# Performance work log

Measured on AMD Instinct MI355X. Metric: run time of the kernel, lower is better.

The kernel has to match this reference:

```python
import jax, jax.numpy as jnp
import numpy as np

ALPHA = 0.2  # LeakyReLU negative slope


def setup_inputs() -> dict:
    key = jax.random.key(0)
    k1, k2, k3, k4 = jax.random.split(key, 4)
    N, IN, OUT = 8192, 512, 256
    x = jax.random.normal(k1, (N, IN), dtype=jnp.float32)
    adj = jnp.zeros((N, N), dtype=jnp.float32)  # accepted but unused by the module
    W = jax.random.normal(k2, (OUT, IN), dtype=jnp.float32) * (1.0 / np.sqrt(IN))
    a1 = jax.random.normal(k3, (OUT,), dtype=jnp.float32) * (1.0 / np.sqrt(OUT))
    a2 = jax.random.normal(k4, (OUT,), dtype=jnp.float32) * (1.0 / np.sqrt(OUT))
    return {"x": x, "adj": adj, "W": W, "a1": a1, "a2": a2}


def reference(x, adj, W, a1, a2):
    # h = tran(x): [N, OUT]
    h = x @ W.T
    # additive GAT scores: e[i, j] = a2 . h_i + a1 . h_j  (from unsqueeze(0)+unsqueeze(1))
    s1 = h @ a1  # [N], att1(h)
    s2 = h @ a2  # [N], att2(h)
    e = s2[:, None] + s1[None, :]  # [N, N]
    e = jnp.where(e > 0, e, ALPHA * e)  # LeakyReLU
    attn = jax.nn.softmax(e, axis=1)  # softmax over dim=1; dropout is identity in eval
    return attn @ h  # [N, OUT]
```

## Files before the change

kernel.cpp:

```cpp
#include <hip/hip_runtime.h>

#define NROW 8192
#define DIN  512
#define DOUT 256
#define NCHUNK 256
#define CLEN 32

constexpr size_t OFF_H      = 0;
constexpr size_t OFF_S1     = OFF_H + (size_t)NROW*DOUT*4;
constexpr size_t OFF_S2     = OFF_S1 + NROW*4;
constexpr size_t OFF_RANK   = OFF_S2 + NROW*4;
constexpr size_t OFF_MISC   = OFF_RANK + NROW*4;
constexpr size_t MEMSET_LEN = OFF_MISC + 256 - OFF_S1;
constexpr size_t OFF_S1S    = OFF_MISC + 256;
constexpr size_t OFF_PERM   = OFF_S1S + NROW*4;
constexpr size_t OFF_WHI    = OFF_PERM + NROW*4;
constexpr size_t OFF_WLO    = OFF_WHI + NROW*4;
constexpr size_t OFF_PRELOS = OFF_WLO + NROW*4;
constexpr size_t OFF_SUFHIS = OFF_PRELOS + 33024;
constexpr size_t OFF_CSLO   = OFF_SUFHIS + 33024;
constexpr size_t OFF_CSHI   = OFF_CSLO + 1024;
constexpr size_t OFF_TLO    = OFF_CSHI + 1024;
constexpr size_t OFF_THI    = OFF_TLO + (size_t)NCHUNK*DOUT*4;
constexpr size_t OFF_PRELO  = OFF_THI + (size_t)NCHUNK*DOUT*4;
constexpr size_t OFF_SUFHI  = OFF_PRELO + (size_t)(NROW+1)*DOUT*4;
constexpr size_t WS_NEED    = OFF_SUFHI + (size_t)(NROW+1)*DOUT*4;

typedef float f32x4 __attribute__((ext_vector_type(4)));
typedef short s16x8 __attribute__((ext_vector_type(8)));
typedef unsigned int u32x4 __attribute__((ext_vector_type(4)));

__device__ __forceinline__ void cvt8_pair(const float4 u, const float4 v,
                                          s16x8& hi, s16x8& lo) {
  float f[8] = {u.x, u.y, u.z, u.w, v.x, v.y, v.z, v.w};
  u32x4 hp, lp;
#pragma unroll
  for (int p = 0; p < 4; ++p) {
    const float f0 = f[2 * p], f1 = f[2 * p + 1];
    const unsigned b0 = __float_as_uint(f0);
    const unsigned b1 = __float_as_uint(f1);
    hp[p] = __builtin_amdgcn_perm(b1, b0, 0x07060302u);
    const float r0 = f0 - __uint_as_float(b0 & 0xffff0000u);
    const float r1 = f1 - __uint_as_float(b1 & 0xffff0000u);
    lp[p] = __builtin_amdgcn_perm(__float_as_uint(r1), __float_as_uint(r0), 0x07060302u);
  }
  hi = __builtin_bit_cast(s16x8, hp);
  lo = __builtin_bit_cast(s16x8, lp);
}

__global__ __launch_bounds__(256) void gemm_h_mfma(const float* __restrict__ x,
                                                   const float* __restrict__ W,
                                                   const float* __restrict__ a1,
                                                   const float* __restrict__ a2,
                                                   float* __restrict__ h,
                                                   float* __restrict__ s1,
                                                   float* __restrict__ s2) {
  __shared__ unsigned short AsH[64][72], AsL[64][72], BsH[64][72], BsL[64][72];
  const int tid = threadIdx.x;
  const int bid = blockIdx.x;
  const int swz = (bid & 7) * 64 + (bid >> 3);
  const int rowBase = (swz >> 2) * 64;
  const int colBase = (swz & 3) * 64;
  const int wid = tid >> 6, lane = tid & 63;
  const int wRow = wid >> 1, wCol = wid & 1;
  const int lhi = lane >> 4, llo = lane & 15;

  f32x4 acc[2][2];
#pragma unroll
  for (int m = 0; m < 2; ++m)
#pragma unroll
    for (int n = 0; n < 2; ++n) acc[m][n] = (f32x4)(0.f);

  const int tr = tid >> 2;
  const int tq = tid & 3;
  const float* px = x + (size_t)(rowBase + tr) * DIN + tq * 16;
  const float* pw = W + (size_t)(colBase + tr) * DIN + tq * 16;

  s16x8 cAh[2], cAl[2], cBh[2], cBl[2];
  {
    float4 a0 = *(const float4*)(px + 0),  a1v = *(const float4*)(px + 4);
    float4 a2v = *(const float4*)(px + 8), a3 = *(const float4*)(px + 12);
    float4 b0 = *(const float4*)(pw + 0),  b1 = *(const float4*)(pw + 4);
    float4 b2 = *(const float4*)(pw + 8),  b3 = *(const float4*)(pw + 12);
    cvt8_pair(a0, a1v, cAh[0], cAl[0]);
    cvt8_pair(a2v, a3, cAh[1], cAl[1]);
    cvt8_pair(b0, b1, cBh[0], cBl[0]);
    cvt8_pair(b2, b3, cBh[1], cBl[1]);
  }

  for (int k0 = 0; k0 < DIN; k0 += 64) {
    __syncthreads();
    *(s16x8*)&AsH[tr][tq * 16 + 0] = cAh[0];
    *(s16x8*)&AsH[tr][tq * 16 + 8] = cAh[1];
    *(s16x8*)&AsL[tr][tq * 16 + 0] = cAl[0];
    *(s16x8*)&AsL[tr][tq * 16 + 8] = cAl[1];
    *(s16x8*)&BsH[tr][tq * 16 + 0] = cBh[0];
    *(s16x8*)&BsH[tr][tq * 16 + 8] = cBh[1];
    *(s16x8*)&BsL[tr][tq * 16 + 0] = cBl[0];
    *(s16x8*)&BsL[tr][tq * 16 + 8] = cBl[1];
    __syncthreads();
    const bool more = (k0 + 64 < DIN);
    float4 a0, a1v, a2v, a3, b0, b1, b2, b3;
    if (more) {
      a0 = *(const float4*)(px + k0 + 64 + 0);  a1v = *(const float4*)(px + k0 + 64 + 4);
      a2v = *(const float4*)(px + k0 + 64 + 8); a3 = *(const float4*)(px + k0 + 64 + 12);
      b0 = *(const float4*)(pw + k0 + 64 + 0);  b1 = *(const float4*)(pw + k0 + 64 + 4);
      b2 = *(const float4*)(pw + k0 + 64 + 8);  b3 = *(const float4*)(pw + k0 + 64 + 12);
    }
#pragma unroll
    for (int kk = 0; kk < 64; kk += 32) {
      s16x8 afh[2], afl[2], bfh[2], bfl[2];
#pragma unroll
      for (int m = 0; m < 2; ++m) {
        afh[m] = *(const s16x8*)&AsH[wRow * 32 + m * 16 + llo][kk + lhi * 8];
        afl[m] = *(const s16x8*)&AsL[wRow * 32 + m * 16 + llo][kk + lhi * 8];
      }
#pragma unroll
      for (int n = 0; n < 2; ++n) {
        bfh[n] = *(const s16x8*)&BsH[wCol * 32 + n * 16 + llo][kk + lhi * 8];
        bfl[n] = *(const s16x8*)&BsL[wCol * 32 + n * 16 + llo][kk + lhi * 8];
      }
#pragma unroll
      for (int m = 0; m < 2; ++m)
#pragma unroll
        for (int n = 0; n < 2; ++n) {
          acc[m][n] = __builtin_amdgcn_mfma_f32_16x16x32_bf16(afh[m], bfh[n], acc[m][n], 0, 0, 0);
          acc[m][n] = __builtin_amdgcn_mfma_f32_16x16x32_bf16(afl[m], bfh[n], acc[m][n], 0, 0, 0);
          acc[m][n] = __builtin_amdgcn_mfma_f32_16x16x32_bf16(afh[m], bfl[n], acc[m][n], 0, 0, 0);
        }
    }
    if (more) {
      cvt8_pair(a0, a1v, cAh[0], cAl[0]);
      cvt8_pair(a2v, a3, cAh[1], cAl[1]);
      cvt8_pair(b0, b1, cBh[0], cBl[0]);
      cvt8_pair(b2, b3, cBh[1], cBl[1]);
    }
  }
  float a1c[2], a2c[2];
#pragma unroll
  for (int n = 0; n < 2; ++n) {
    const int col = colBase + wCol * 32 + n * 16 + llo;
    a1c[n] = a1[col];
    a2c[n] = a2[col];
  }
#pragma unroll
  for (int m = 0; m < 2; ++m) {
    float p1[4] = {0.f, 0.f, 0.f, 0.f}, p2[4] = {0.f, 0.f, 0.f, 0.f};
#pragma unroll
    for (int n = 0; n < 2; ++n) {
      const int col = colBase + wCol * 32 + n * 16 + llo;
#pragma unroll
      for (int j = 0; j < 4; ++j) {
        const int row = rowBase + wRow * 32 + m * 16 + lhi * 4 + j;
        h[(size_t)row * DOUT + col] = acc[m][n][j];
        p1[j] = fmaf(acc[m][n][j], a1c[n], p1[j]);
        p2[j] = fmaf(acc[m][n][j], a2c[n], p2[j]);
      }
    }
#pragma unroll
    for (int j = 0; j < 4; ++j) {
#pragma unroll
      for (int msk = 1; msk < 16; msk <<= 1) {
        p1[j] += __shfl_xor(p1[j], msk);
        p2[j] += __shfl_xor(p2[j], msk);
      }
    }
    if (llo == 0) {
#pragma unroll
      for (int j = 0; j < 4; ++j) {
        const int row = rowBase + wRow * 32 + m * 16 + lhi * 4 + j;
        atomicAdd(&s1[row], p1[j]);
        atomicAdd(&s2[row], p2[j]);
      }
    }
  }
}

__global__ __launch_bounds__(256) void rank_count(const float* __restrict__ s1,
                                                  int* __restrict__ rank,
                                                  unsigned int* __restrict__ miscu) {
  __shared__ float sj[1024];
  __shared__ float wm[4];
  const int t = threadIdx.x;
  const int ib = blockIdx.x, jc = blockIdx.y;
  const int j0 = jc * 1024;
  *(float4*)&sj[t << 2] = *(const float4*)(s1 + j0 + (t << 2));
  const int i = ib * 256 + t;
  const float v = s1[i];
  __syncthreads();
  int cnt = 0;
#pragma unroll 4
  for (int q = 0; q < 256; ++q) {
    float4 sv = *(const float4*)&sj[q << 2];
    int jg = j0 + (q << 2);
    cnt += (int)(sv.x < v) + (int)((sv.x == v) & (jg + 0 < i));
    cnt += (int)(sv.y < v) + (int)((sv.y == v) & (jg + 1 < i));
    cnt += (int)(sv.z < v) + (int)((sv.z == v) & (jg + 2 < i));
    cnt += (int)(sv.w < v) + (int)((sv.w == v) & (jg + 3 < i));
  }
  atomicAdd(&rank[i], cnt);
  if (jc == 0) {
    float m = v;
#pragma unroll
    for (int off = 32; off > 0; off >>= 1) m = fmaxf(m, __shfl_down(m, off));
    if ((t & 63) == 0) wm[t >> 6] = m;
    __syncthreads();
    if (t == 0) {
      float mm = fmaxf(fmaxf(wm[0], wm[1]), fmaxf(wm[2], wm[3]));
      unsigned int b = __float_as_uint(mm);
      unsigned int enc = (b & 0x80000000u) ? ~b : (b | 0x80000000u);
      atomicMax(miscu, enc);
    }
  }
}

__global__ __launch_bounds__(256) void scatter_w(const float* __restrict__ s1,
                                                 const int* __restrict__ rank,
                                                 const unsigned int* __restrict__ miscu,
                                                 float* __restrict__ miscf,
                                                 float* __restrict__ s1s,
                                                 int* __restrict__ perm,
                                                 float* __restrict__ w_hi,
                                                 float* __restrict__ w_lo) {
  const int i = blockIdx.x * 256 + threadIdx.x;
  unsigned int e = miscu[0];
  unsigned int b = (e & 0x80000000u) ? (e & 0x7fffffffu) : ~e;
  const float M1 = __uint_as_float(b);
  const float v = s1[i];
  const int r = rank[i];
  s1s[r] = v;
  perm[r] = i;
  w_hi[r] = __expf(v - M1);
  w_lo[r] = __expf(0.2f * (v - M1));
  if (i == 0) miscf[0] = M1;
}

__global__ __launch_bounds__(256) void chunk_totals(const float* __restrict__ h,
                                                    const int* __restrict__ perm,
                                                    const float* __restrict__ w_hi,
                                                    const float* __restrict__ w_lo,
                                                    float* __restrict__ T_lo,
                                                    float* __restrict__ T_hi,
                                                    float* __restrict__ cs_lo,
                                                    float* __restrict__ cs_hi) {
  const int d = threadIdx.x, b = blockIdx.x;
  const int j0 = b * CLEN;
  float tlo = 0.f, thi = 0.f;
#pragma unroll
  for (int e = 0; e < CLEN; e += 4) {
    int4 p4 = *(const int4*)(perm + j0 + e);
    float4 wl4 = *(const float4*)(w_lo + j0 + e);
    float4 wh4 = *(const float4*)(w_hi + j0 + e);
    float h0 = h[(size_t)p4.x * DOUT + d];
    float h1 = h[(size_t)p4.y * DOUT + d];
    float h2 = h[(size_t)p4.z * DOUT + d];
    float h3 = h[(size_t)p4.w * DOUT + d];
    tlo += wl4.x * h0 + wl4.y * h1 + wl4.z * h2 + wl4.w * h3;
    thi += wh4.x * h0 + wh4.y * h1 + wh4.z * h2 + wh4.w * h3;
  }
  T_lo[b * DOUT + d] = tlo;
  T_hi[b * DOUT + d] = thi;
  if (d < 64) {
    float wl = (d < 32) ? w_lo[j0 + d] : 0.f;
    float wh = (d < 32) ? w_hi[j0 + d] : 0.f;
#pragma unroll
    for (int off = 32; off > 0; off >>= 1) {
      wl += __shfl_down(wl, off);
      wh += __shfl_down(wh, off);
    }
    if (d == 0) { cs_lo[b] = wl; cs_hi[b] = wh; }
  }
}

__global__ __launch_bounds__(256) void write_prefix(const float* __restrict__ h,
                                                    const int* __restrict__ perm,
                                                    const float* __restrict__ w_hi,
                                                    const float* __restrict__ w_lo,
                                                    const float* __restrict__ T_lo,
                                                    const float* __restrict__ T_hi,
                                                    const float* __restrict__ cs_lo,
                                                    const float* __restrict__ cs_hi,
                                                    float* __restrict__ PreLo,
                                                    float* __restrict__ SufHi,
                                                    float* __restrict__ prelo_s,
                                                    float* __restrict__ sufhi_s) {
  const int d = threadIdx.x, b = blockIdx.x;
  const int j0 = b * CLEN;
  if (d < 64) {
    float accp = 0.f, acct = 0.f;
    for (int p = d; p < NCHUNK; p += 64) {
      float cl = cs_lo[p], ch = cs_hi[p];
      accp += (p < b) ? cl : 0.f;
      acct += (p > b) ? ch : 0.f;
    }
#pragma unroll
    for (int off = 32; off > 0; off >>= 1) {
      accp += __shfl_down(accp, off);
      acct += __shfl_down(acct, off);
    }
    float pres  = __shfl(accp, 0);
    float tails = __shfl(acct, 0);
    float wl = (d < 32) ? w_lo[j0 + d] : 0.f;
    float wh = (d < 32) ? w_hi[j0 + d] : 0.f;
    float pl = wl, ph = wh;
#pragma unroll
    for (int off = 1; off < 32; off <<= 1) {
      float a = __shfl_up(pl, off);
      float c = __shfl_up(ph, off);
      if (d >= off) { pl += a; ph += c; }
    }
    float chunk_hi_tot = __shfl(ph, 31);
    if (d < 32) {
      prelo_s[j0 + d] = pres + (pl - wl);
      sufhi_s[j0 + d] = tails + (chunk_hi_tot - (ph - wh));
    }
    if (b == NCHUNK - 1 && d == 31) {
      prelo_s[NROW] = pres + pl;
      sufhi_s[NROW] = 0.f;
    }
  }
  float rl = 0.f, tail = 0.f;
#pragma unroll 4
  for (int p = 0; p < b; ++p)           rl   += T_lo[p * DOUT + d];
#pragma unroll 4
  for (int p = b + 1; p < NCHUNK; ++p)  tail += T_hi[p * DOUT + d];
  float phl[CLEN], phh[CLEN];
  float ownHi = 0.f;
#pragma unroll
  for (int e = 0; e < CLEN; e += 4) {
    int4 p4 = *(const int4*)(perm + j0 + e);
    float4 wl4 = *(const float4*)(w_lo + j0 + e);
    float4 wh4 = *(const float4*)(w_hi + j0 + e);
    float h0 = h[(size_t)p4.x * DOUT + d];
    float h1 = h[(size_t)p4.y * DOUT + d];
    float h2 = h[(size_t)p4.z * DOUT + d];
    float h3 = h[(size_t)p4.w * DOUT + d];
    phl[e + 0] = wl4.x * h0; phl[e + 1] = wl4.y * h1;
    phl[e + 2] = wl4.z * h2; phl[e + 3] = wl4.w * h3;
    phh[e + 0] = wh4.x * h0; phh[e + 1] = wh4.y * h1;
    phh[e + 2] = wh4.z * h2; phh[e + 3] = wh4.w * h3;
    ownHi += phh[e + 0] + phh[e + 1] + phh[e + 2] + phh[e + 3];
  }
  float shb = tail + ownHi;
  float preh = 0.f;
#pragma unroll
  for (int e = 0; e < CLEN; ++e) {
    size_t j = (size_t)(j0 + e);
    PreLo[j * DOUT + d] = rl;
    SufHi[j * DOUT + d] = shb - preh;
    rl   += phl[e];
    preh += phh[e];
  }
  if (b == NCHUNK - 1) {
    PreLo[(size_t)NROW * DOUT + d] = rl;
    SufHi[(size_t)NROW * DOUT + d] = 0.f;
  }
}

__global__ __launch_bounds__(256) void finalize(const float* __restrict__ s2,
                                                const float* __restrict__ s1s,
                                                const float* __restrict__ miscf,
                                                const float* __restrict__ PreLo,
                                                const float* __restrict__ SufHi,
                                                const float* __restrict__ prelo_s,
                                                const float* __restrict__ sufhi_s,
                                                float* __restrict__ out) {
  const int wave = threadIdx.x >> 6, lane = threadIdx.x & 63;
  const int i = blockIdx.x * 4 + wave;
  const float c = s2[i];
  const float M1 = miscf[0];
  const float tval = -c;
  int lo = 0, hi = NROW;
  while (lo < hi) {
    int mid = (lo + hi) >> 1;
    if (s1s[mid] <= tval) lo = mid + 1; else hi = mid;
  }
  const int k = lo;
  const float u = c + M1;
  const float m = fmaxf(u, 0.2f * u);
  const float fh = __expf(u - m);
  const float fl = __expf(0.2f * u - m);
  const float den = fh * sufhi_s[k] + fl * prelo_s[k];
  const float inv = 1.f / den;
  float4 A = *(const float4*)(SufHi + (size_t)k * DOUT + (lane << 2));
  float4 B = *(const float4*)(PreLo + (size_t)k * DOUT + (lane << 2));
  float4 o;
  o.x = (fh * A.x + fl * B.x) * inv;
  o.y = (fh * A.y + fl * B.y) * inv;
  o.z = (fh * A.z + fl * B.z) * inv;
  o.w = (fh * A.w + fl * B.w) * inv;
  *(float4*)(out + (size_t)i * DOUT + (lane << 2)) = o;
}

extern "C" void kernel_launch(void* const* d_in, const int* in_sizes, int n_in,
                              void* d_out, int out_size, void* d_ws, size_t ws_size,
                              hipStream_t stream) {
  const float* x  = (const float*)d_in[0];
  const float* W  = (const float*)d_in[2];
  const float* a1 = (const float*)d_in[3];
  const float* a2 = (const float*)d_in[4];
  float* out = (float*)d_out;

  char* ws = (char*)d_ws;
  if (ws_size < WS_NEED) ws = (char*)d_in[1];

  float*          h       = (float*)(ws + OFF_H);
  float*          s1      = (float*)(ws + OFF_S1);
  float*          s2      = (float*)(ws + OFF_S2);
  int*            rank    = (int*)  (ws + OFF_RANK);
  unsigned int*   miscu   = (unsigned int*)(ws + OFF_MISC);
  float*          miscf   = (float*)(ws + OFF_MISC) + 1;
  float*          s1s     = (float*)(ws + OFF_S1S);
  int*            perm    = (int*)  (ws + OFF_PERM);
  float*          w_hi    = (float*)(ws + OFF_WHI);
  float*          w_lo    = (float*)(ws + OFF_WLO);
  float*          prelo_s = (float*)(ws + OFF_PRELOS);
  float*          sufhi_s = (float*)(ws + OFF_SUFHIS);
  float*          cs_lo   = (float*)(ws + OFF_CSLO);
  float*          cs_hi   = (float*)(ws + OFF_CSHI);
  float*          T_lo    = (float*)(ws + OFF_TLO);
  float*          T_hi    = (float*)(ws + OFF_THI);
  float*          PreLo   = (float*)(ws + OFF_PRELO);
  float*          SufHi   = (float*)(ws + OFF_SUFHI);

  hipMemsetAsync(s1, 0, MEMSET_LEN, stream);

  gemm_h_mfma<<<512, 256, 0, stream>>>(x, W, a1, a2, h, s1, s2);
  rank_count<<<dim3(NROW / 256, 8), 256, 0, stream>>>(s1, rank, miscu);
  scatter_w<<<NROW / 256, 256, 0, stream>>>(s1, rank, miscu, miscf, s1s, perm, w_hi, w_lo);
  chunk_totals<<<NCHUNK, 256, 0, stream>>>(h, perm, w_hi, w_lo, T_lo, T_hi, cs_lo, cs_hi);
  write_prefix<<<NCHUNK, 256, 0, stream>>>(h, perm, w_hi, w_lo, T_lo, T_hi, cs_lo, cs_hi,
                                           PreLo, SufHi, prelo_s, sufhi_s);
  finalize<<<NROW / 4, 256, 0, stream>>>(s2, s1s, miscf, PreLo, SufHi, prelo_s, sufhi_s, out);
}
```

Baseline: 381.8 us.

## Fuse post-GEMM stages into one cooperative kernel with grid syncs

```diff
diff --git a/kernel.cpp b/kernel.cpp
--- a/kernel.cpp
+++ b/kernel.cpp
@@ -1,4 +1,7 @@
 #include <hip/hip_runtime.h>
+#include <hip/hip_cooperative_groups.h>
+
+namespace cg = cooperative_groups;
 
 #define NROW 8192
 #define DIN  512
@@ -172,6 +175,218 @@
         atomicAdd(&s1[row], p1[j]);
         atomicAdd(&s2[row], p2[j]);
       }
+    }
+  }
+}
+
+__global__ __launch_bounds__(256) void backend(const float* __restrict__ s1,
+                                               const float* __restrict__ s2,
+                                               int* __restrict__ rank,
+                                               unsigned int* __restrict__ miscu,
+                                               float* __restrict__ miscf,
+                                               float* __restrict__ s1s,
+                                               int* __restrict__ perm,
+                                               float* __restrict__ w_hi,
+                                               float* __restrict__ w_lo,
+                                               const float* __restrict__ h,
+                                               float* __restrict__ T_lo,
+                                               float* __restrict__ T_hi,
+                                               float* __restrict__ cs_lo,
+                                               float* __restrict__ cs_hi,
+                                               float* __restrict__ PreLo,
+                                               float* __restrict__ SufHi,
+                                               float* __restrict__ prelo_s,
+                                               float* __restrict__ sufhi_s,
+                                               float* __restrict__ out) {
+  cg::grid_group grid = cg::this_grid();
+  __shared__ float sjA[512];
+  __shared__ float wm[4];
+  const int t = threadIdx.x;
+  const int b = blockIdx.x;
+
+  {
+    const int ib = b >> 4, jc = b & 15;
+    const int j0 = jc * 512;
+    if (t < 128) *(float4*)&sjA[t << 2] = *(const float4*)(s1 + j0 + (t << 2));
+    const int i = ib * 256 + t;
+    const float v = s1[i];
+    __syncthreads();
+    int cnt = 0;
+#pragma unroll 4
+    for (int q = 0; q < 128; ++q) {
+      float4 sv = *(const float4*)&sjA[q << 2];
+      int jg = j0 + (q << 2);
+      cnt += (int)(sv.x < v) + (int)((sv.x == v) & (jg + 0 < i));
+      cnt += (int)(sv.y < v) + (int)((sv.y == v) & (jg + 1 < i));
+      cnt += (int)(sv.z < v) + (int)((sv.z == v) & (jg + 2 < i));
+      cnt += (int)(sv.w < v) + (int)((sv.w == v) & (jg + 3 < i));
+    }
+    atomicAdd(&rank[i], cnt);
+    if (jc == 0) {
+      float m = v;
+#pragma unroll
+      for (int off = 32; off > 0; off >>= 1) m = fmaxf(m, __shfl_down(m, off));
+      if ((t & 63) == 0) wm[t >> 6] = m;
+      __syncthreads();
+      if (t == 0) {
+        float mm = fmaxf(fmaxf(wm[0], wm[1]), fmaxf(wm[2], wm[3]));
+        unsigned int bb = __float_as_uint(mm);
+        unsigned int enc = (bb & 0x80000000u) ? ~bb : (bb | 0x80000000u);
+        atomicMax(miscu, enc);
+      }
+    }
+  }
+  grid.sync();
+
+  if (b < 32) {
+    const int i = b * 256 + t;
+    unsigned int e = miscu[0];
+    unsigned int bb = (e & 0x80000000u) ? (e & 0x7fffffffu) : ~e;
+    const float M1 = __uint_as_float(bb);
+    const float v = s1[i];
+    const int r = rank[i];
+    s1s[r] = v;
+    perm[r] = i;
+    w_hi[r] = __expf(v - M1);
+    w_lo[r] = __expf(0.2f * (v - M1));
+    if (i == 0) miscf[0] = M1;
+  }
+  grid.sync();
+
+  if (b < NCHUNK) {
+    const int d = t;
+    const int j0 = b * CLEN;
+    float tlo = 0.f, thi = 0.f;
+#pragma unroll
+    for (int e = 0; e < CLEN; e += 4) {
+      int4 p4 = *(const int4*)(perm + j0 + e);
+      float4 wl4 = *(const float4*)(w_lo + j0 + e);
+      float4 wh4 = *(const float4*)(w_hi + j0 + e);
+      float h0 = h[(size_t)p4.x * DOUT + d];
+      float h1 = h[(size_t)p4.y * DOUT + d];
+      float h2 = h[(size_t)p4.z * DOUT + d];
+      float h3 = h[(size_t)p4.w * DOUT + d];
+      tlo += wl4.x * h0 + wl4.y * h1 + wl4.z * h2 + wl4.w * h3;
+      thi += wh4.x * h0 + wh4.y * h1 + wh4.z * h2 + wh4.w * h3;
+    }
+    T_lo[b * DOUT + d] = tlo;
+    T_hi[b * DOUT + d] = thi;
+    if (d < 64) {
+      float wl = (d < 32) ? w_lo[j0 + d] : 0.f;
+      float wh = (d < 32) ? w_hi[j0 + d] : 0.f;
+#pragma unroll
+      for (int off = 32; off > 0; off >>= 1) {
+        wl += __shfl_down(wl, off);
+        wh += __shfl_down(wh, off);
+      }
+      if (d == 0) { cs_lo[b] = wl; cs_hi[b] = wh; }
+    }
+  }
+  grid.sync();
+
+  if (b < NCHUNK) {
+    const int d = t;
+    const int j0 = b * CLEN;
+    if (d < 64) {
+      float accp = 0.f, acct = 0.f;
+      for (int p = d; p < NCHUNK; p += 64) {
+        float cl = cs_lo[p], ch = cs_hi[p];
+        accp += (p < b) ? cl : 0.f;
+        acct += (p > b) ? ch : 0.f;
+      }
+#pragma unroll
+      for (int off = 32; off > 0; off >>= 1) {
+        accp += __shfl_down(accp, off);
+        acct += __shfl_down(acct, off);
+      }
+      float pres  = __shfl(accp, 0);
+      float tails = __shfl(acct, 0);
+      float wl = (d < 32) ? w_lo[j0 + d] : 0.f;
+      float wh = (d < 32) ? w_hi[j0 + d] : 0.f;
+      float pl = wl, ph = wh;
+#pragma unroll
+      for (int off = 1; off < 32; off <<= 1) {
+        float a = __shfl_up(pl, off);
+        float c = __shfl_up(ph, off);
+        if (d >= off) { pl += a; ph += c; }
+      }
+      float chunk_hi_tot = __shfl(ph, 31);
+      if (d < 32) {
+        prelo_s[j0 + d] = pres + (pl - wl);
+        sufhi_s[j0 + d] = tails + (chunk_hi_tot - (ph - wh));
+      }
+      if (b == NCHUNK - 1 && d == 31) {
+        prelo_s[NROW] = pres + pl;
+        sufhi_s[NROW] = 0.f;
+      }
+    }
+    float rl = 0.f, tail = 0.f;
+#pragma unroll 4
+    for (int p = 0; p < b; ++p)           rl   += T_lo[p * DOUT + d];
+#pragma unroll 4
+    for (int p = b + 1; p < NCHUNK; ++p)  tail += T_hi[p * DOUT + d];
+    float phl[CLEN], phh[CLEN];
+    float ownHi = 0.f;
+#pragma unroll
+    for (int e = 0; e < CLEN; e += 4) {
+      int4 p4 = *(const int4*)(perm + j0 + e);
+      float4 wl4 = *(const float4*)(w_lo + j0 + e);
+      float4 wh4 = *(const float4*)(w_hi + j0 + e);
+      float h0 = h[(size_t)p4.x * DOUT + d];
+      float h1 = h[(size_t)p4.y * DOUT + d];
+      float h2 = h[(size_t)p4.z * DOUT + d];
+      float h3 = h[(size_t)p4.w * DOUT + d];
+      phl[e + 0] = wl4.x * h0; phl[e + 1] = wl4.y * h1;
+      phl[e + 2] = wl4.z * h2; phl[e + 3] = wl4.w * h3;
+      phh[e + 0] = wh4.x * h0; phh[e + 1] = wh4.y * h1;
+      phh[e + 2] = wh4.z * h2; phh[e + 3] = wh4.w * h3;
+      ownHi += phh[e + 0] + phh[e + 1] + phh[e + 2] + phh[e + 3];
+    }
+    float shb = tail + ownHi;
+    float preh = 0.f;
+#pragma unroll
+    for (int e = 0; e < CLEN; ++e) {
+      size_t j = (size_t)(j0 + e);
+      PreLo[j * DOUT + d] = rl;
+      SufHi[j * DOUT + d] = shb - preh;
+      rl   += phl[e];
+      preh += phh[e];
+    }
+    if (b == NCHUNK - 1) {
+      PreLo[(size_t)NROW * DOUT + d] = rl;
+      SufHi[(size_t)NROW * DOUT + d] = 0.f;
+    }
+  }
+  grid.sync();
+
+  {
+    const int wave = t >> 6, lane = t & 63;
+    const float M1 = miscf[0];
+#pragma unroll
+    for (int rep = 0; rep < 4; ++rep) {
+      const int i = b * 16 + wave * 4 + rep;
+      const float c = s2[i];
+      const float tval = -c;
+      int lo = 0, hi = NROW;
+      while (lo < hi) {
+        int mid = (lo + hi) >> 1;
+        if (s1s[mid] <= tval) lo = mid + 1; else hi = mid;
+      }
+      const int k = lo;
+      const float u = c + M1;
+      const float m = fmaxf(u, 0.2f * u);
+      const float fh = __expf(u - m);
+      const float fl = __expf(0.2f * u - m);
+      const float den = fh * sufhi_s[k] + fl * prelo_s[k];
+      const float inv = 1.f / den;
+      float4 A = *(const float4*)(SufHi + (size_t)k * DOUT + (lane << 2));
+      float4 B = *(const float4*)(PreLo + (size_t)k * DOUT + (lane << 2));
+      float4 o;
+      o.x = (fh * A.x + fl * B.x) * inv;
+      o.y = (fh * A.y + fl * B.y) * inv;
+      o.z = (fh * A.z + fl * B.z) * inv;
+      o.w = (fh * A.w + fl * B.w) * inv;
+      *(float4*)(out + (size_t)i * DOUT + (lane << 2)) = o;
     }
   }
 }
@@ -426,10 +641,23 @@
   hipMemsetAsync(s1, 0, MEMSET_LEN, stream);
 
   gemm_h_mfma<<<512, 256, 0, stream>>>(x, W, a1, a2, h, s1, s2);
-  rank_count<<<dim3(NROW / 256, 8), 256, 0, stream>>>(s1, rank, miscu);
-  scatter_w<<<NROW / 256, 256, 0, stream>>>(s1, rank, miscu, miscf, s1s, perm, w_hi, w_lo);
-  chunk_totals<<<NCHUNK, 256, 0, stream>>>(h, perm, w_hi, w_lo, T_lo, T_hi, cs_lo, cs_hi);
-  write_prefix<<<NCHUNK, 256, 0, stream>>>(h, perm, w_hi, w_lo, T_lo, T_hi, cs_lo, cs_hi,
-                                           PreLo, SufHi, prelo_s, sufhi_s);
-  finalize<<<NROW / 4, 256, 0, stream>>>(s2, s1s, miscf, PreLo, SufHi, prelo_s, sufhi_s, out);
-}
+
+  const float* s1c = s1;
+  const float* s2c = s2;
+  const float* hc  = h;
+  void* args[] = {(void*)&s1c, (void*)&s2c, (void*)&rank, (void*)&miscu, (void*)&miscf,
+                  (void*)&s1s, (void*)&perm, (void*)&w_hi, (void*)&w_lo,
+                  (void*)&hc, (void*)&T_lo, (void*)&T_hi, (void*)&cs_lo, (void*)&cs_hi,
+                  (void*)&PreLo, (void*)&SufHi, (void*)&prelo_s, (void*)&sufhi_s,
+                  (void*)&out};
+  hipError_t err = hipLaunchCooperativeKernel((void*)backend, dim3(512), dim3(256),
+                                              args, 0, stream);
+  if (err != hipSuccess) {
+    rank_count<<<dim3(NROW / 256, 8), 256, 0, stream>>>(s1, rank, miscu);
+    scatter_w<<<NROW / 256, 256, 0, stream>>>(s1, rank, miscu, miscf, s1s, perm, w_hi, w_lo);
+    chunk_totals<<<NCHUNK, 256, 0, stream>>>(h, perm, w_hi, w_lo, T_lo, T_hi, cs_lo, cs_hi);
+    write_prefix<<<NCHUNK, 256, 0, stream>>>(h, perm, w_hi, w_lo, T_lo, T_hi, cs_lo, cs_hi,
+                                             PreLo, SufHi, prelo_s, sufhi_s);
+    finalize<<<NROW / 4, 256, 0, stream>>>(s2, s1s, miscf, PreLo, SufHi, prelo_s, sufhi_s, out);
+  }
+}
```

Result: slower. 570.3 us (+49.4%).
